# Performance work log

Measured on AMD Instinct MI355X. Metric: run time of the kernel, lower is better.

## Reference

```python
import jax, jax.numpy as jnp
import numpy as np

N, E, H, T = 50000, 100000, 512, 6  # nodes, edges, hidden_size, num_edge_types


def setup_inputs() -> dict:
    key = jax.random.key(0)
    ks = jax.random.split(key, 14)
    xav = 1.0 / np.sqrt(H)
    return {
        "statement_embeddings": jax.random.normal(ks[0], (N, H), jnp.float32),
        "source_indices": jax.random.randint(ks[1], (E,), 0, N, dtype=jnp.int32),
        "dest_indices": jax.random.randint(ks[2], (E,), 0, N, dtype=jnp.int32),
        "edge_types": jax.random.randint(ks[3], (E,), 0, T, dtype=jnp.int32),
        "num_nodes": N,
        "hidden_size": H,
        # edge_dense: Dense(features=6*H), xavier_uniform kernel, tiny-normal bias
        "W_edge": jax.random.uniform(ks[4], (H, T * H), jnp.float32, -1.0, 1.0) * np.sqrt(6.0 / (H + T * H)),
        "b_edge": jax.random.normal(ks[5], (T * H,), jnp.float32) * 1e-6,
        # GRUCell params (flax convention: input denses have bias; hidden r/z denses no bias; hidden n dense has bias)
        "W_ir": jax.random.normal(ks[6], (H, H), jnp.float32) * xav,
        "W_iz": jax.random.normal(ks[7], (H, H), jnp.float32) * xav,
        "W_in": jax.random.normal(ks[8], (H, H), jnp.float32) * xav,
        "b_ir": jnp.zeros((H,), jnp.float32),
        "b_iz": jnp.zeros((H,), jnp.float32),
        "b_in": jnp.zeros((H,), jnp.float32),
        "W_hr": jax.random.normal(ks[9], (H, H), jnp.float32) * xav,
        "W_hz": jax.random.normal(ks[10], (H, H), jnp.float32) * xav,
        "W_hn": jax.random.normal(ks[11], (H, H), jnp.float32) * xav,
        "b_hn": jnp.zeros((H,), jnp.float32),
    }


def reference(statement_embeddings, source_indices, dest_indices, edge_types,
              num_nodes, hidden_size,
              W_edge, b_edge,
              W_ir, W_iz, W_in, b_ir, b_iz, b_in,
              W_hr, W_hz, W_hn, b_hn):
    num_edge_types = 6
    # gather source node embeddings: [E, H]
    src = statement_embeddings[source_indices]
    # per-edge dense to all edge types: [E, T*H] -> [E, T, H]
    all_types = (src @ W_edge + b_edge).reshape(-1, num_edge_types, hidden_size)
    # select the slice for each edge's type: [E, H]
    msgs = jnp.take_along_axis(all_types, edge_types[:, None, None], axis=1)[:, 0, :]
    # scatter-add to destination nodes: [N, H]
    proposed = jax.ops.segment_sum(msgs, dest_indices, num_segments=num_nodes)
    # GRU update: inputs=proposed, carry=statement_embeddings
    h = statement_embeddings
    r = jax.nn.sigmoid(proposed @ W_ir + b_ir + h @ W_hr)
    z = jax.nn.sigmoid(proposed @ W_iz + b_iz + h @ W_hz)
    n = jnp.tanh(proposed @ W_in + b_in + r * (h @ W_hn + b_hn))
    return (1.0 - z) * n + z * h
```

## Files before the change

kernel.cpp:

```cpp
#include <hip/hip_runtime.h>
#include <hip/hip_bf16.h>
#include <math.h>

#define H 512
#define NT 6

#define EBM 128
#define EBN 256
#define EBK 32
#define GBM 128
#define GBN 64
#define GBK 32

#define PSCALE 65536.0f
#define PINV   (1.0f / 65536.0f)

typedef short bf16x8 __attribute__((ext_vector_type(8)));
typedef float f32x4 __attribute__((ext_vector_type(4)));

__device__ __forceinline__ float sigmoidf_(float x) { return 1.0f / (1.0f + expf(-x)); }

__device__ __forceinline__ unsigned short f2bf(float f) {
    unsigned int u = __float_as_uint(f);
    u = (u + 0x7FFF + ((u >> 16) & 1)) >> 16;
    return (unsigned short)u;
}

__device__ __forceinline__ void glds16(const void* g, void* l) {
    __builtin_amdgcn_global_load_lds((const __attribute__((address_space(1))) unsigned int*)g,
                                     (__attribute__((address_space(3))) unsigned int*)l,
                                     16, 0, 0);
}

#define WAITBAR(N)                                                        \
    {                                                                     \
        asm volatile("s_waitcnt vmcnt(" #N ") lgkmcnt(0)" ::: "memory");  \
        __builtin_amdgcn_s_barrier();                                     \
        asm volatile("" ::: "memory");                                    \
    }

__device__ __forceinline__ void xcd_colmajor_map(int gx, int gy, int* rowT, int* colT) {
    const int nwg = gx * gy;
    const int bid = (int)(blockIdx.y * gridDim.x + blockIdx.x);
    const int x = bid & 7;
    const int o = bid >> 3;
    const int q = nwg >> 3, rr = nwg & 7;
    const int L = (x < rr) ? x * (q + 1) + o : rr * (q + 1) + (x - rr) * q + o;
    *colT = L / gy;
    *rowT = L % gy;
}

__global__ void hist_kernel(const int* __restrict__ etype, int E, int* __restrict__ meta) {
    __shared__ int lh[NT];
    if (threadIdx.x < NT) lh[threadIdx.x] = 0;
    __syncthreads();
    int i = blockIdx.x * blockDim.x + threadIdx.x;
    if (i < E) atomicAdd(&lh[etype[i]], 1);
    __syncthreads();
    if (threadIdx.x < NT) {
        int c = lh[threadIdx.x];
        if (c) atomicAdd(&meta[threadIdx.x], c);
    }
}

__global__ void prefix_kernel(int* __restrict__ meta) {
    if (threadIdx.x == 0 && blockIdx.x == 0) {
        int acc = 0;
        for (int t = 0; t < NT; ++t) {
            meta[8 + t]  = acc;
            meta[16 + t] = acc;
            acc += ((meta[t] + EBM - 1) / EBM) * EBM;
        }
        meta[8 + NT] = acc;
    }
}

__global__ void scatter_perm_kernel(const int* __restrict__ etype, int E,
                                    int* __restrict__ meta, int* __restrict__ perm) {
    __shared__ int lcount[NT];
    __shared__ int lbase[NT];
    const int tid = threadIdx.x;
    if (tid < NT) lcount[tid] = 0;
    __syncthreads();
    int i = blockIdx.x * blockDim.x + tid;
    int t = 0, rank = 0;
    if (i < E) {
        t = etype[i];
        rank = atomicAdd(&lcount[t], 1);
    }
    __syncthreads();
    if (tid < NT) {
        int c = lcount[tid];
        lbase[tid] = c ? atomicAdd(&meta[16 + tid], c) : 0;
    }
    __syncthreads();
    if (i < E) perm[lbase[t] + rank] = i;
}

__global__ void conv_to_ah(const float* __restrict__ in, unsigned short* __restrict__ AH,
                           int n4, int half) {
    int i = blockIdx.x * blockDim.x + threadIdx.x;
    if (i < n4) {
        float4 v = ((const float4*)in)[i];
        ushort4 o;
        o.x = f2bf(v.x); o.y = f2bf(v.y); o.z = f2bf(v.z); o.w = f2bf(v.w);
        int row = i >> 7;
        int c4  = i & 127;
        ((ushort4*)AH)[row * 256 + half * 128 + c4] = o;
    }
}

__global__ void conv_i2ah(const int* __restrict__ in, unsigned short* __restrict__ AH, int n4) {
    int i = blockIdx.x * blockDim.x + threadIdx.x;
    if (i < n4) {
        int4 v = ((const int4*)in)[i];
        ushort4 o;
        o.x = f2bf((float)v.x * PINV); o.y = f2bf((float)v.y * PINV);
        o.z = f2bf((float)v.z * PINV); o.w = f2bf((float)v.w * PINV);
        int row = i >> 7;
        int c4  = i & 127;
        ((ushort4*)AH)[row * 256 + c4] = o;
    }
}

__global__ void conv_gru_w_kernel(const float* __restrict__ Wir, const float* __restrict__ Wiz,
                                  const float* __restrict__ Win, const float* __restrict__ Whr,
                                  const float* __restrict__ Whz, const float* __restrict__ Whn,
                                  unsigned short* __restrict__ Brt, unsigned short* __restrict__ Bzt,
                                  unsigned short* __restrict__ Bnt) {
    int idx = blockIdx.x * blockDim.x + threadIdx.x;
    if (idx >= 512 * 1024) return;
    int n = idx >> 10;
    int k = idx & 1023;
    int kk = k & 511;
    const float* wr = (k < 512) ? Wir : Whr;
    const float* wz = (k < 512) ? Wiz : Whz;
    const float* wn = (k < 512) ? Win : Whn;
    Brt[idx] = f2bf(wr[kk * H + n]);
    Bzt[idx] = f2bf(wz[kk * H + n]);
    Bnt[idx] = f2bf(wn[kk * H + n]);
}

__global__ void conv_edge_w_kernel(const float* __restrict__ W_edge, unsigned short* __restrict__ WeT) {
    int idx = blockIdx.x * blockDim.x + threadIdx.x;
    if (idx >= 3072 * 512) return;
    int n = idx >> 9;
    int k = idx & 511;
    WeT[idx] = f2bf(W_edge[(size_t)k * (NT * H) + n]);
}

__global__ __launch_bounds__(256, 2)
void edge_msg_mfma(const unsigned short* __restrict__ AH,
                   const int* __restrict__ src_idx,
                   const int* __restrict__ dst_idx,
                   const float* __restrict__ b_edge,
                   const unsigned short* __restrict__ WeT,
                   const int* __restrict__ meta,
                   const int* __restrict__ perm,
                   int* __restrict__ proposed)
{
    __shared__ short As[3][EBM * EBK];
    __shared__ short Bs[3][EBN * EBK];
    __shared__ int ls_src[EBM];
    __shared__ int ls_dst[EBM];

    int rowT, colT;
    xcd_colmajor_map(gridDim.x, gridDim.y, &rowT, &colT);
    const int rowBase = rowT * EBM;
    if (rowBase >= meta[8 + NT]) return;
    int t = 0;
    while (rowBase >= meta[8 + t + 1]) ++t;

    const int colBase = colT * EBN;
    const int tid = threadIdx.x;

    if (tid < EBM) {
        int e = perm[rowBase + tid];
        int s = 512, d = -1;
        if (e >= 0) { s = src_idx[e] * 1024 + 512; d = dst_idx[e] * H; }
        ls_src[tid] = s;
        ls_dst[tid] = d;
    }
    __syncthreads();

    const int lane = tid & 63;
    const int wave = tid >> 6;
    const int wm = (wave >> 1) * 64;
    const int wn = (wave & 1) * 128;
    const int q = lane >> 4;
    const int r = lane & 15;

    const int rA = tid >> 2;
    const int gs = (((tid & 3) ^ ((rA >> 1) & 3)) * 8);
    const int qs8 = ((q ^ ((r >> 1) & 3)) * 8);

    const size_t s0 = (size_t)ls_src[rA] + gs;
    const size_t s1 = (size_t)ls_src[64 + rA] + gs;
    const size_t bB = ((size_t)(t * H + colBase + rA)) * H + gs;

    f32x4 acc[4][8];
    #pragma unroll
    for (int i = 0; i < 4; ++i)
        #pragma unroll
        for (int j = 0; j < 8; ++j) acc[i][j] = (f32x4){0.f, 0.f, 0.f, 0.f};

#define ESTAGE(S, B)                                                          \
    {                                                                         \
        glds16(AH + s0 + (S) * EBK, &As[B][tid * 8]);                         \
        glds16(AH + s1 + (S) * EBK, &As[B][(256 + tid) * 8]);                 \
        glds16(WeT + bB + (S) * EBK,                 &Bs[B][tid * 8]);        \
        glds16(WeT + bB + 64 * H + (S) * EBK,  &Bs[B][(256 + tid) * 8]);      \
        glds16(WeT + bB + 128 * H + (S) * EBK, &Bs[B][(512 + tid) * 8]);      \
        glds16(WeT + bB + 192 * H + (S) * EBK, &Bs[B][(768 + tid) * 8]);      \
    }

#define ECOMPUTE(B)                                                                               \
    {                                                                                             \
        bf16x8 a[4];                                                                              \
        _Pragma("unroll")                                                                         \
        for (int i = 0; i < 4; ++i)                                                               \
            a[i] = *(const bf16x8*)&As[B][(wm + i * 16 + r) * EBK + qs8];                         \
        _Pragma("unroll")                                                                         \
        for (int j = 0; j < 8; ++j) {                                                             \
            bf16x8 b = *(const bf16x8*)&Bs[B][(wn + j * 16 + r) * EBK + qs8];                     \
            _Pragma("unroll")                                                                     \
            for (int i = 0; i < 4; ++i)                                                           \
                acc[i][j] = __builtin_amdgcn_mfma_f32_16x16x32_bf16(a[i], b, acc[i][j], 0, 0, 0); \
        }                                                                                         \
    }

    ESTAGE(0, 0);
    ESTAGE(1, 1);
    for (int s = 0; s < 14; ++s) {
        WAITBAR(6);
        ESTAGE(s + 2, (s + 2) % 3);
        ECOMPUTE(s % 3);
    }
    { WAITBAR(6); ECOMPUTE(2); }
    { WAITBAR(0); ECOMPUTE(0); }
#undef ESTAGE
#undef ECOMPUTE

    int cols[8];
    float bias[8];
    #pragma unroll
    for (int j = 0; j < 8; ++j) {
        cols[j] = colBase + wn + j * 16 + r;
        bias[j] = b_edge[t * H + cols[j]];
    }
    #pragma unroll
    for (int i = 0; i < 4; ++i) {
        #pragma unroll
        for (int reg = 0; reg < 4; ++reg) {
            int row = wm + i * 16 + q * 4 + reg;
            int d = ls_dst[row];
            if (d < 0) continue;
            #pragma unroll
            for (int j = 0; j < 8; ++j)
                atomicAdd(&proposed[(size_t)d + cols[j]],
                          __float2int_rn((acc[i][j][reg] + bias[j]) * PSCALE));
        }
    }
}

__global__ __launch_bounds__(256, 2)
void gru_mfma(const unsigned short* __restrict__ AH,
              const float* __restrict__ emb_f32,
              const unsigned short* __restrict__ Brt,
              const unsigned short* __restrict__ Bzt,
              const unsigned short* __restrict__ Bnt,
              const float* __restrict__ bir, const float* __restrict__ biz,
              const float* __restrict__ bin, const float* __restrict__ bhn,
              float* __restrict__ out, int N)
{
    __shared__ short As[3][GBM * GBK];
    __shared__ short Brs[3][GBN * GBK];
    __shared__ short Bzs[3][GBN * GBK];
    __shared__ short Bns[3][GBN * GBK];

    int rowT, colT;
    xcd_colmajor_map(gridDim.x, gridDim.y, &rowT, &colT);
    const int rowBase = rowT * GBM;
    const int colBase = colT * GBN;

    const int tid = threadIdx.x;
    const int lane = tid & 63;
    const int wave = tid >> 6;
    const int wm = (wave >> 1) * 64;
    const int wn = (wave & 1) * 32;
    const int q = lane >> 4;
    const int r = lane & 15;

    const int rA = tid >> 2;
    const int gs = (((tid & 3) ^ ((rA >> 1) & 3)) * 8);
    const int qs8 = ((q ^ ((r >> 1) & 3)) * 8);

    const size_t aOff0 = (size_t)(rowBase + rA) * 1024 + gs;
    const size_t aOff1 = (size_t)(rowBase + 64 + rA) * 1024 + gs;
    const size_t bOff  = (size_t)(colBase + rA) * 1024 + gs;

    f32x4 accR[4][2], accZ[4][2], accNI[4][2], accNH[4][2];
    #pragma unroll
    for (int i = 0; i < 4; ++i)
        #pragma unroll
        for (int j = 0; j < 2; ++j) {
            accR[i][j] = (f32x4){0.f, 0.f, 0.f, 0.f};
            accZ[i][j] = accR[i][j];
            accNI[i][j] = accR[i][j];
            accNH[i][j] = accR[i][j];
        }

#define GSTAGE(S, B)                                             \
    {                                                            \
        glds16(AH + aOff0 + (S) * GBK, &As[B][tid * 8]);         \
        glds16(AH + aOff1 + (S) * GBK, &As[B][(256 + tid) * 8]); \
        glds16(Brt + bOff + (S) * GBK, &Brs[B][tid * 8]);        \
        glds16(Bzt + bOff + (S) * GBK, &Bzs[B][tid * 8]);        \
        glds16(Bnt + bOff + (S) * GBK, &Bns[B][tid * 8]);        \
    }

#define GCOMPUTE(ACCN, B)                                                                            \
    {                                                                                                \
        bf16x8 a[4];                                                                                 \
        _Pragma("unroll")                                                                            \
        for (int i = 0; i < 4; ++i)                                                                  \
            a[i] = *(const bf16x8*)&As[B][(wm + i * 16 + r) * GBK + qs8];                            \
        _Pragma("unroll")                                                                            \
        for (int j = 0; j < 2; ++j) {                                                                \
            bf16x8 br = *(const bf16x8*)&Brs[B][(wn + j * 16 + r) * GBK + qs8];                      \
            bf16x8 bz = *(const bf16x8*)&Bzs[B][(wn + j * 16 + r) * GBK + qs8];                      \
            bf16x8 bn = *(const bf16x8*)&Bns[B][(wn + j * 16 + r) * GBK + qs8];                      \
            _Pragma("unroll")                                                                        \
            for (int i = 0; i < 4; ++i) {                                                            \
                accR[i][j] = __builtin_amdgcn_mfma_f32_16x16x32_bf16(a[i], br, accR[i][j], 0, 0, 0); \
                accZ[i][j] = __builtin_amdgcn_mfma_f32_16x16x32_bf16(a[i], bz, accZ[i][j], 0, 0, 0); \
                ACCN[i][j] = __builtin_amdgcn_mfma_f32_16x16x32_bf16(a[i], bn, ACCN[i][j], 0, 0, 0); \
            }                                                                                        \
        }                                                                                            \
    }

#define GSTEP(S, ACCN)                   \
    {                                    \
        WAITBAR(5);                      \
        GSTAGE((S) + 2, ((S) + 2) % 3);  \
        GCOMPUTE(ACCN, (S) % 3);         \
    }

    GSTAGE(0, 0);
    GSTAGE(1, 1);
    GSTEP(0,  accNI) GSTEP(1,  accNI) GSTEP(2,  accNI) GSTEP(3,  accNI)
    GSTEP(4,  accNI) GSTEP(5,  accNI) GSTEP(6,  accNI) GSTEP(7,  accNI)
    GSTEP(8,  accNI) GSTEP(9,  accNI) GSTEP(10, accNI) GSTEP(11, accNI)
    GSTEP(12, accNI) GSTEP(13, accNI) GSTEP(14, accNI) GSTEP(15, accNI)
    GSTEP(16, accNH) GSTEP(17, accNH) GSTEP(18, accNH) GSTEP(19, accNH)
    GSTEP(20, accNH) GSTEP(21, accNH) GSTEP(22, accNH) GSTEP(23, accNH)
    GSTEP(24, accNH) GSTEP(25, accNH) GSTEP(26, accNH) GSTEP(27, accNH)
    GSTEP(28, accNH) GSTEP(29, accNH)
    { WAITBAR(5); GCOMPUTE(accNH, 0); }
    { WAITBAR(0); GCOMPUTE(accNH, 1); }
#undef GSTAGE
#undef GCOMPUTE
#undef GSTEP

    #pragma unroll
    for (int j = 0; j < 2; ++j) {
        const int col = colBase + wn + j * 16 + r;
        const float vbir = bir[col], vbiz = biz[col], vbin = bin[col], vbhn = bhn[col];
        #pragma unroll
        for (int i = 0; i < 4; ++i) {
            #pragma unroll
            for (int reg = 0; reg < 4; ++reg) {
                const int row = rowBase + wm + i * 16 + q * 4 + reg;
                if (row >= N) continue;
                float rg = sigmoidf_(accR[i][j][reg] + vbir);
                float zg = sigmoidf_(accZ[i][j][reg] + vbiz);
                float ng = tanhf(accNI[i][j][reg] + vbin + rg * (accNH[i][j][reg] + vbhn));
                float h = emb_f32[(size_t)row * H + col];
                out[(size_t)row * H + col] = (1.0f - zg) * ng + zg * h;
            }
        }
    }
}

extern "C" void kernel_launch(void* const* d_in, const int* in_sizes, int n_in,
                              void* d_out, int out_size, void* d_ws, size_t ws_size,
                              hipStream_t stream) {
    const float* emb     = (const float*)d_in[0];
    const int*   src_idx = (const int*)d_in[1];
    const int*   dst_idx = (const int*)d_in[2];
    const int*   etype   = (const int*)d_in[3];
    const float* W_edge  = (const float*)d_in[6];
    const float* b_edge  = (const float*)d_in[7];
    const float* Wir = (const float*)d_in[8];
    const float* Wiz = (const float*)d_in[9];
    const float* Win = (const float*)d_in[10];
    const float* bir = (const float*)d_in[11];
    const float* biz = (const float*)d_in[12];
    const float* bin = (const float*)d_in[13];
    const float* Whr = (const float*)d_in[14];
    const float* Whz = (const float*)d_in[15];
    const float* Whn = (const float*)d_in[16];
    const float* bhn = (const float*)d_in[17];

    const int E = in_sizes[1];
    const int N = in_sizes[0] / H;
    const int NH = N * H;

    char* ws = (char*)d_ws;
    int*            proposed = (int*)ws;                         ws += (size_t)NH * 4;
    unsigned short* AH       = (unsigned short*)ws;              ws += (size_t)NH * 2 * 2;
    unsigned short* Brt      = (unsigned short*)ws;              ws += 512 * 1024 * 2;
    unsigned short* Bzt      = (unsigned short*)ws;              ws += 512 * 1024 * 2;
    unsigned short* Bnt      = (unsigned short*)ws;              ws += 512 * 1024 * 2;
    unsigned short* WeT      = (unsigned short*)ws;              ws += 3072 * 512 * 2;
    int*            meta     = (int*)ws;                         ws += 32 * 4;
    int*            perm     = (int*)ws;
    const int maxRowTiles = (E + EBM - 1) / EBM + NT;

    hipMemsetAsync(proposed, 0, (size_t)NH * 4, stream);
    hipMemsetAsync(meta, 0, 32 * 4, stream);
    hipMemsetAsync(perm, 0xFF, (size_t)maxRowTiles * EBM * 4, stream);

    const int n4 = NH / 4;
    conv_to_ah<<<(n4 + 255) / 256, 256, 0, stream>>>(emb, AH, n4, 1);
    conv_gru_w_kernel<<<(512 * 1024 + 255) / 256, 256, 0, stream>>>(
        Wir, Wiz, Win, Whr, Whz, Whn, Brt, Bzt, Bnt);
    conv_edge_w_kernel<<<(3072 * 512 + 255) / 256, 256, 0, stream>>>(W_edge, WeT);

    hist_kernel<<<(E + 255) / 256, 256, 0, stream>>>(etype, E, meta);
    prefix_kernel<<<1, 64, 0, stream>>>(meta);
    scatter_perm_kernel<<<(E + 255) / 256, 256, 0, stream>>>(etype, E, meta, perm);

    dim3 egrid(H / EBN, maxRowTiles);
    edge_msg_mfma<<<egrid, 256, 0, stream>>>(AH, src_idx, dst_idx, b_edge, WeT,
                                             meta, perm, proposed);

    conv_i2ah<<<(n4 + 255) / 256, 256, 0, stream>>>(proposed, AH, n4);

    dim3 ggrid(H / GBN, (N + GBM - 1) / GBM);
    gru_mfma<<<ggrid, 256, 0, stream>>>(AH, emb, Brt, Bzt, Bnt,
                                        bir, biz, bin, bhn, (float*)d_out, N);
}
```

Before: 803.1 us.

## Interleave GRU tile loads with MFMA halves and switch to row-band tile mapping

The GRU GEMM main loop is restructured so each K-step issues its prefetch loads in two groups. Each group is interleaved with half of the MFMA work, using extra barriers, s_setprio and sched_barrier to overlap memory issue with matrix math. Separately, the workgroup-to-tile mapping for both the edge-message and GRU kernels changes from column-major to row-band order, which alters L2 reuse patterns. The extra barriers per step add synchronisation cost, and the new mapping may reduce reuse of weight tiles.

```diff
diff --git a/kernel.cpp b/kernel.cpp
--- a/kernel.cpp
+++ b/kernel.cpp
@@ -39,15 +39,15 @@
         asm volatile("" ::: "memory");                                    \
     }
 
-__device__ __forceinline__ void xcd_colmajor_map(int gx, int gy, int* rowT, int* colT) {
+__device__ __forceinline__ void xcd_rowband_map(int gx, int gy, int* rowT, int* colT) {
     const int nwg = gx * gy;
     const int bid = (int)(blockIdx.y * gridDim.x + blockIdx.x);
     const int x = bid & 7;
     const int o = bid >> 3;
     const int q = nwg >> 3, rr = nwg & 7;
     const int L = (x < rr) ? x * (q + 1) + o : rr * (q + 1) + (x - rr) * q + o;
-    *colT = L / gy;
-    *rowT = L % gy;
+    *rowT = L / gx;
+    *colT = L % gx;
 }
 
 __global__ void hist_kernel(const int* __restrict__ etype, int E, int* __restrict__ meta) {
@@ -165,7 +165,7 @@
     __shared__ int ls_dst[EBM];
 
     int rowT, colT;
-    xcd_colmajor_map(gridDim.x, gridDim.y, &rowT, &colT);
+    xcd_rowband_map(gridDim.x, gridDim.y, &rowT, &colT);
     const int rowBase = rowT * EBM;
     if (rowBase >= meta[8 + NT]) return;
     int t = 0;
@@ -279,7 +279,7 @@
     __shared__ short Bns[3][GBN * GBK];
 
     int rowT, colT;
-    xcd_colmajor_map(gridDim.x, gridDim.y, &rowT, &colT);
+    xcd_rowband_map(gridDim.x, gridDim.y, &rowT, &colT);
     const int rowBase = rowT * GBM;
     const int colBase = colT * GBN;
 
@@ -319,48 +319,78 @@
         glds16(Bnt + bOff + (S) * GBK, &Bns[B][tid * 8]);        \
     }
 
-#define GCOMPUTE(ACCN, B)                                                                            \
-    {                                                                                                \
-        bf16x8 a[4];                                                                                 \
-        _Pragma("unroll")                                                                            \
-        for (int i = 0; i < 4; ++i)                                                                  \
-            a[i] = *(const bf16x8*)&As[B][(wm + i * 16 + r) * GBK + qs8];                            \
-        _Pragma("unroll")                                                                            \
-        for (int j = 0; j < 2; ++j) {                                                                \
-            bf16x8 br = *(const bf16x8*)&Brs[B][(wn + j * 16 + r) * GBK + qs8];                      \
-            bf16x8 bz = *(const bf16x8*)&Bzs[B][(wn + j * 16 + r) * GBK + qs8];                      \
-            bf16x8 bn = *(const bf16x8*)&Bns[B][(wn + j * 16 + r) * GBK + qs8];                      \
-            _Pragma("unroll")                                                                        \
-            for (int i = 0; i < 4; ++i) {                                                            \
-                accR[i][j] = __builtin_amdgcn_mfma_f32_16x16x32_bf16(a[i], br, accR[i][j], 0, 0, 0); \
-                accZ[i][j] = __builtin_amdgcn_mfma_f32_16x16x32_bf16(a[i], bz, accZ[i][j], 0, 0, 0); \
-                ACCN[i][j] = __builtin_amdgcn_mfma_f32_16x16x32_bf16(a[i], bn, ACCN[i][j], 0, 0, 0); \
-            }                                                                                        \
-        }                                                                                            \
-    }
-
-#define GSTEP(S, ACCN)                   \
+#define GSTEP8(S, ACCN, DOSTAGE)                                                                       \
+    {                                                                                                  \
+        const int B_ = (S) % 3;                                                                        \
+        const int W_ = ((S) + 2) % 3;                                                                  \
+        bf16x8 a_[4];                                                                                  \
+                         \
+        _Pragma("unroll")                                                                              \
+        for (int i = 0; i < 4; ++i)                                                                    \
+            a_[i] = *(const bf16x8*)&As[B_][(wm + i * 16 + r) * GBK + qs8];                            \
+        bf16x8 br0 = *(const bf16x8*)&Brs[B_][(wn + r) * GBK + qs8];                                   \
+        bf16x8 bz0 = *(const bf16x8*)&Bzs[B_][(wn + r) * GBK + qs8];                                   \
+        bf16x8 bn0 = *(const bf16x8*)&Bns[B_][(wn + r) * GBK + qs8];                                   \
+        if (DOSTAGE) {                                                                                 \
+            glds16(AH + aOff0 + ((S) + 2) * GBK, &As[W_][tid * 8]);                                    \
+            glds16(AH + aOff1 + ((S) + 2) * GBK, &As[W_][(256 + tid) * 8]);                            \
+            glds16(Brt + bOff + ((S) + 2) * GBK, &Brs[W_][tid * 8]);                                   \
+        }                                                                                              \
+        __builtin_amdgcn_s_barrier();                                                                  \
+        asm volatile("s_waitcnt lgkmcnt(0)" ::: "memory");                                             \
+        __builtin_amdgcn_sched_barrier(0);                                                             \
+        __builtin_amdgcn_s_setprio(1);                                                                 \
+        _Pragma("unroll")                                                                              \
+        for (int i = 0; i < 4; ++i) {                                                                  \
+            accR[i][0] = __builtin_amdgcn_mfma_f32_16x16x32_bf16(a_[i], br0, accR[i][0], 0, 0, 0);     \
+            accZ[i][0] = __builtin_amdgcn_mfma_f32_16x16x32_bf16(a_[i], bz0, accZ[i][0], 0, 0, 0);     \
+            ACCN[i][0] = __builtin_amdgcn_mfma_f32_16x16x32_bf16(a_[i], bn0, ACCN[i][0], 0, 0, 0);     \
+        }                                                                                              \
+        __builtin_amdgcn_s_setprio(0);                                                                 \
+        __builtin_amdgcn_s_barrier();                                                                  \
+                                      \
+        bf16x8 br1 = *(const bf16x8*)&Brs[B_][(wn + 16 + r) * GBK + qs8];                              \
+        bf16x8 bz1 = *(const bf16x8*)&Bzs[B_][(wn + 16 + r) * GBK + qs8];                              \
+        bf16x8 bn1 = *(const bf16x8*)&Bns[B_][(wn + 16 + r) * GBK + qs8];                              \
+        if (DOSTAGE) {                                                                                 \
+            glds16(Bzt + bOff + ((S) + 2) * GBK, &Bzs[W_][tid * 8]);                                   \
+            glds16(Bnt + bOff + ((S) + 2) * GBK, &Bns[W_][tid * 8]);                                   \
+        }                                                                                              \
+        __builtin_amdgcn_s_barrier();                                                                  \
+        asm volatile("s_waitcnt lgkmcnt(0)" ::: "memory");                                             \
+        __builtin_amdgcn_sched_barrier(0);                                                             \
+        __builtin_amdgcn_s_setprio(1);                                                                 \
+        _Pragma("unroll")                                                                              \
+        for (int i = 0; i < 4; ++i) {                                                                  \
+            accR[i][1] = __builtin_amdgcn_mfma_f32_16x16x32_bf16(a_[i], br1, accR[i][1], 0, 0, 0);     \
+            accZ[i][1] = __builtin_amdgcn_mfma_f32_16x16x32_bf16(a_[i], bz1, accZ[i][1], 0, 0, 0);     \
+            ACCN[i][1] = __builtin_amdgcn_mfma_f32_16x16x32_bf16(a_[i], bn1, ACCN[i][1], 0, 0, 0);     \
+        }                                                                                              \
+        __builtin_amdgcn_s_setprio(0);                                                                 \
+                                \
+    }
+
+#define GFULL(S, ACCN)                   \
     {                                    \
         WAITBAR(5);                      \
-        GSTAGE((S) + 2, ((S) + 2) % 3);  \
-        GCOMPUTE(ACCN, (S) % 3);         \
+        GSTEP8(S, ACCN, 1);              \
     }
 
     GSTAGE(0, 0);
     GSTAGE(1, 1);
-    GSTEP(0,  accNI) GSTEP(1,  accNI) GSTEP(2,  accNI) GSTEP(3,  accNI)
-    GSTEP(4,  accNI) GSTEP(5,  accNI) GSTEP(6,  accNI) GSTEP(7,  accNI)
-    GSTEP(8,  accNI) GSTEP(9,  accNI) GSTEP(10, accNI) GSTEP(11, accNI)
-    GSTEP(12, accNI) GSTEP(13, accNI) GSTEP(14, accNI) GSTEP(15, accNI)
-    GSTEP(16, accNH) GSTEP(17, accNH) GSTEP(18, accNH) GSTEP(19, accNH)
-    GSTEP(20, accNH) GSTEP(21, accNH) GSTEP(22, accNH) GSTEP(23, accNH)
-    GSTEP(24, accNH) GSTEP(25, accNH) GSTEP(26, accNH) GSTEP(27, accNH)
-    GSTEP(28, accNH) GSTEP(29, accNH)
-    { WAITBAR(5); GCOMPUTE(accNH, 0); }
-    { WAITBAR(0); GCOMPUTE(accNH, 1); }
+    GFULL(0,  accNI) GFULL(1,  accNI) GFULL(2,  accNI) GFULL(3,  accNI)
+    GFULL(4,  accNI) GFULL(5,  accNI) GFULL(6,  accNI) GFULL(7,  accNI)
+    GFULL(8,  accNI) GFULL(9,  accNI) GFULL(10, accNI) GFULL(11, accNI)
+    GFULL(12, accNI) GFULL(13, accNI) GFULL(14, accNI) GFULL(15, accNI)
+    GFULL(16, accNH) GFULL(17, accNH) GFULL(18, accNH) GFULL(19, accNH)
+    GFULL(20, accNH) GFULL(21, accNH) GFULL(22, accNH) GFULL(23, accNH)
+    GFULL(24, accNH) GFULL(25, accNH) GFULL(26, accNH) GFULL(27, accNH)
+    GFULL(28, accNH) GFULL(29, accNH)
+    { WAITBAR(5); GSTEP8(30, accNH, 0); }
+    { WAITBAR(0); GSTEP8(31, accNH, 0); }
 #undef GSTAGE
-#undef GCOMPUTE
-#undef GSTEP
+#undef GSTEP8
+#undef GFULL
 
     #pragma unroll
     for (int j = 0; j < 2; ++j) {
```

Result: no change. 793.1 us (-1.2%).
